# Kernel tuning notes

Measured on AMD Instinct MI355X. Metric: run time of the kernel, lower is better.

Reference implementation:

```python
import jax, jax.numpy as jnp
import numpy as np

N = 8192
DIN = 256
DOUT = 128
ALPHA = 0.2      # leaky-relu negative slope
K_MAX = 32       # static upper bound on action.max()+1 (action in [0, 32))
NEG_BIG = -9.0e15


def setup_inputs() -> dict:
    key = jax.random.key(0)
    ks = jax.random.split(key, 6)
    xavier_w = 1.414 * np.sqrt(6.0 / (DIN + DOUT))
    xavier_a = 1.414 * np.sqrt(6.0 / (DOUT + 1))
    return {
        "input": jax.random.normal(ks[0], (N, DIN), dtype=jnp.float32),
        "adj": jax.random.randint(ks[1], (N, N), 0, 2, dtype=jnp.int32),
        "action": jax.random.randint(ks[2], (N,), 0, K_MAX, dtype=jnp.int32),
        "W": jax.random.uniform(ks[3], (DIN, DOUT), jnp.float32, -xavier_w, xavier_w),
        "a_self": jax.random.uniform(ks[4], (DOUT, 1), jnp.float32, -xavier_a, xavier_a),
        "a_neighs": jax.random.uniform(ks[5], (DOUT, 1), jnp.float32, -xavier_a, xavier_a),
        "breadth_policy": 1,
    }


def reference(input, adj, action, W, a_self, a_neighs, breadth_policy):
    h = input @ W                                  # [N, DOUT]
    attn_self = h @ a_self                         # [N, 1]
    attn_neighs = h @ a_neighs                     # [N, 1]
    e = jax.nn.leaky_relu(attn_self + attn_neighs.T, negative_slope=ALPHA)  # [N, N]
    masked = jnp.where(adj > 0, e, jnp.float32(NEG_BIG))
    attention = jax.nn.softmax(masked, axis=1)     # [N, N]
    if breadth_policy:
        # static K_MAX >= action.max()+1; thresholds only read index action[i]
        top_vals, _ = jax.lax.top_k(attention, K_MAX)          # [N, K_MAX], sorted desc
        thresholds = top_vals[jnp.arange(N), action]           # [N]
        attention = jnp.where(attention < thresholds[:, None], 0.0, attention)
    h_prime = attention @ h                        # [N, DOUT]
    return jax.nn.elu(h_prime)                     # concat=True
```

## Files before the change

kernel.cpp:

```cpp
#include <hip/hip_runtime.h>
#include <cstdint>
#include <cstddef>

#define NN    8192
#define DIN   256
#define DOUT  128
#define LRA   0.2f

__global__ __launch_bounds__(256) void gemm_st_kernel(
    const float* __restrict__ input, const float* __restrict__ W,
    const float* __restrict__ a_self, const float* __restrict__ a_neighs,
    float* __restrict__ h, float* __restrict__ s_arr,
    float* __restrict__ t_arr)
{
    __shared__ float tile[16][DIN];
    __shared__ float pr[4][16];
    const int tid  = threadIdx.x;
    const int row0 = blockIdx.x * 16;
    {
        const float4* in4 = (const float4*)(input + (size_t)row0 * DIN);
        float4* t4 = (float4*)&tile[0][0];
        #pragma unroll
        for (int k = 0; k < 4; ++k) t4[tid + k * 256] = in4[tid + k * 256];
    }
    __syncthreads();
    const int c    = tid & 127;
    const int g    = tid >> 7;
    const int lane = tid & 63;
    const int wave = tid >> 6;
    float acc[8];
    #pragma unroll
    for (int m = 0; m < 8; ++m) acc[m] = 0.f;
    for (int k = 0; k < DIN; k += 4) {
        const float w0 = W[(k + 0) * DOUT + c];
        const float w1 = W[(k + 1) * DOUT + c];
        const float w2 = W[(k + 2) * DOUT + c];
        const float w3 = W[(k + 3) * DOUT + c];
        #pragma unroll
        for (int m = 0; m < 8; ++m) {
            const float4 av = *(const float4*)&tile[g * 8 + m][k];
            acc[m] += av.x * w0 + av.y * w1 + av.z * w2 + av.w * w3;
        }
    }
    #pragma unroll
    for (int m = 0; m < 8; ++m)
        h[(size_t)(row0 + g * 8 + m) * DOUT + c] = acc[m];

    const float as = a_self[c];
    const float an = a_neighs[c];
    #pragma unroll
    for (int m = 0; m < 8; ++m) {
        float vs = acc[m] * as;
        float vt = acc[m] * an;
        for (int off = 32; off > 0; off >>= 1) {
            vs += __shfl_down(vs, off);
            vt += __shfl_down(vt, off);
        }
        if (lane == 0) { pr[wave][2 * m] = vs; pr[wave][2 * m + 1] = vt; }
    }
    __syncthreads();
    if (tid < 16) {
        const int m  = tid & 7;
        const int gg = tid >> 3;
        const int r  = row0 + gg * 8 + m;
        s_arr[r] = pr[2 * gg][2 * m]     + pr[2 * gg + 1][2 * m];
        t_arr[r] = pr[2 * gg][2 * m + 1] + pr[2 * gg + 1][2 * m + 1];
    }
}

__global__ __launch_bounds__(256) void rank_kernel(
    const float* __restrict__ t, int* __restrict__ order,
    float* __restrict__ tsorted)
{
    __shared__ float tl[NN];
    __shared__ int   part[8][32];
    for (int k = threadIdx.x; k < NN; k += 256) tl[k] = t[k];
    __syncthreads();
    const int jloc = threadIdx.x & 31;
    const int seg  = threadIdx.x >> 5;
    const int j    = blockIdx.x * 32 + jloc;
    const float tj = tl[j];
    int r = 0;
    const int k0 = seg * (NN / 8);
    for (int i = 0; i < NN / 8; ++i) {
        const int k = k0 + ((i + seg * 4) & (NN / 8 - 1));
        const float tk = tl[k];
        r += (tk > tj || (tk == tj && k < j)) ? 1 : 0;
    }
    part[seg][jloc] = r;
    __syncthreads();
    if (threadIdx.x < 32) {
        int rr = 0;
        #pragma unroll
        for (int ss = 0; ss < 8; ++ss) rr += part[ss][threadIdx.x];
        const int jj = blockIdx.x * 32 + threadIdx.x;
        order[rr]   = jj;
        tsorted[rr] = tl[jj];
    }
}

__global__ __launch_bounds__(256) void gat_row_kernel(
    const int* __restrict__ adj, const float* __restrict__ s_arr,
    const float* __restrict__ t_arr, const int* __restrict__ order,
    const float* __restrict__ tsorted, const int* __restrict__ action,
    const float* __restrict__ h, const int* __restrict__ policy,
    float* __restrict__ out)
{
    __shared__ float red[4];
    __shared__ float numlds[8][DOUT];
    __shared__ unsigned long long maskb[32][4];
    __shared__ int   sel_j[64];
    __shared__ float sel_w[64];
    __shared__ int   sel_cnt_sh;
    __shared__ int   done_sh;

    const int row  = blockIdx.x;
    const int tid  = threadIdx.x;
    const int lane = tid & 63;
    const int wave = tid >> 6;

    const float s    = s_arr[row];
    const float tmax = tsorted[0];
    const float zc   = s + tmax;
    const float C    = fmaxf(zc, LRA * zc);

    const int4*   arow = (const int4*)(adj + (size_t)row * NN);
    const float4* t4   = (const float4*)t_arr;
    float acc = 0.f;
    #pragma unroll
    for (int k = 0; k < 8; ++k) {
        const int idx = tid + k * 256;
        const int4   a  = arow[idx];
        const float4 tv = t4[idx];
        const int vx = a.x > 0, vy = a.y > 0, vz = a.z > 0, vw = a.w > 0;
        float z, e;
        z = s + tv.x; e = fmaxf(z, LRA * z); if (vx) acc += __expf(e - C);
        z = s + tv.y; e = fmaxf(z, LRA * z); if (vy) acc += __expf(e - C);
        z = s + tv.z; e = fmaxf(z, LRA * z); if (vz) acc += __expf(e - C);
        z = s + tv.w; e = fmaxf(z, LRA * z); if (vw) acc += __expf(e - C);
        const unsigned long long b0 = __ballot(vx);
        const unsigned long long b1 = __ballot(vy);
        const unsigned long long b2 = __ballot(vz);
        const unsigned long long b3 = __ballot(vw);
        if (lane == 0) {
            const int ch = 4 * k + wave;
            maskb[ch][0] = b0; maskb[ch][1] = b1;
            maskb[ch][2] = b2; maskb[ch][3] = b3;
        }
    }
    for (int off = 32; off > 0; off >>= 1) acc += __shfl_down(acc, off);
    if (lane == 0) red[wave] = acc;
    __syncthreads();
    const float l = red[0] + red[1] + red[2] + red[3];

    int K = action[row] + 1;
    if (policy[0] == 0) K = 0x7FFFFFFF;
    const int ee = tid >> 5;
    const int c4 = tid & 31;
    float4 acc4 = make_float4(0.f, 0.f, 0.f, 0.f);
    float tthr = -3.0e38f;
    int found = 0, cnt = 0, base = 0;

    while (true) {
        if (tid < 64) {
            const int p = base + lane;
            int j = 0, valid = 0;
            float tjv = -3.0e38f;
            if (p < NN) {
                j     = order[p];
                tjv   = tsorted[p];
                valid = (int)((maskb[j >> 8][j & 3] >> ((j & 255) >> 2)) & 1ull);
            }
            const unsigned long long vm = __ballot(valid);
            if (!found) {
                const int cv = __popcll(vm);
                if (cnt + cv >= K) {
                    const int need = K - cnt;
                    const int myrank =
                        __popcll(vm & ((1ull << lane) - 1ull)) + 1;
                    const unsigned long long pm =
                        __ballot(valid && (myrank == need));
                    const int L = __ffsll((long long)pm) - 1;
                    tthr  = __shfl(tjv, L);
                    found = 1;
                } else {
                    cnt += cv;
                }
            }
            const int selected = valid && (tjv >= tthr);
            const unsigned long long sm = __ballot(selected);
            const int pos = __popcll(sm & ((1ull << lane) - 1ull));
            if (selected) {
                const float z = s + tjv;
                const float e = fmaxf(z, LRA * z);
                sel_j[pos] = j;
                sel_w[pos] = __expf(e - C);
            }
            if (lane == 0) {
                sel_cnt_sh = __popcll(sm);
                const int nb = base + 64;
                int dn;
                if (nb >= NN)   dn = 1;
                else if (found) dn = (tsorted[nb] < tthr) ? 1 : 0;
                else            dn = 0;
                done_sh = dn;
            }
        }
        __syncthreads();
        const int nsel = sel_cnt_sh;
        const int dn   = done_sh;
        for (int e2 = ee; e2 < nsel; e2 += 8) {
            const float w = sel_w[e2];
            const float4 hv =
                *(const float4*)&h[(size_t)sel_j[e2] * DOUT + c4 * 4];
            acc4.x += w * hv.x; acc4.y += w * hv.y;
            acc4.z += w * hv.z; acc4.w += w * hv.w;
        }
        base += 64;
        if (dn) break;
        __syncthreads();
    }

    *(float4*)&numlds[ee][c4 * 4] = acc4;
    __syncthreads();
    if (tid < DOUT) {
        float v = 0.f;
        #pragma unroll
        for (int q = 0; q < 8; ++q) v += numlds[q][tid];
        v /= l;
        out[(size_t)row * DOUT + tid] = (v > 0.f) ? v : expm1f(v);
    }
}

extern "C" void kernel_launch(void* const* d_in, const int* in_sizes, int n_in,
                              void* d_out, int out_size, void* d_ws,
                              size_t ws_size, hipStream_t stream)
{
    const float* input    = (const float*)d_in[0];
    const int*   adj      = (const int*)d_in[1];
    const int*   action   = (const int*)d_in[2];
    const float* W        = (const float*)d_in[3];
    const float* a_self   = (const float*)d_in[4];
    const float* a_neighs = (const float*)d_in[5];
    const int*   policy   = (const int*)d_in[6];
    float* out = (float*)d_out;

    float* ws      = (float*)d_ws;
    float* h       = ws;
    float* s       = ws + (size_t)NN * DOUT;
    float* t       = s + NN;
    float* tsorted = t + NN;
    int*   order   = (int*)(tsorted + NN);

    hipLaunchKernelGGL(gemm_st_kernel, dim3(512), dim3(256), 0, stream,
                       input, W, a_self, a_neighs, h, s, t);
    hipLaunchKernelGGL(rank_kernel, dim3(256), dim3(256), 0, stream,
                       t, order, tsorted);
    hipLaunchKernelGGL(gat_row_kernel, dim3(NN), dim3(256), 0, stream,
                       adj, s, t, order, tsorted, action, h, policy, out);
}
```

Before: 459.6 us.

## Split row kernel into denominator pass and one-wave-per-row top-k walk

The fused per-row kernel is split in two. The first kernel streams adj, computes the softmax denominator and writes the adjacency bitmask to global memory. The second kernel handles one row per 64-lane wave, using shuffles instead of LDS and block barriers, and walks the sorted candidates to gather h. The aim is to stop three idle waves per block from waiting on barriers during the serial walk. The cost is an extra launch plus a global round trip for the mask (8192x1KB) and the denominators.

```diff
diff --git a/kernel.cpp b/kernel.cpp
--- a/kernel.cpp
+++ b/kernel.cpp
@@ -99,21 +99,12 @@
     }
 }
 
-__global__ __launch_bounds__(256) void gat_row_kernel(
+__global__ __launch_bounds__(256) void denom_kernel(
     const int* __restrict__ adj, const float* __restrict__ s_arr,
-    const float* __restrict__ t_arr, const int* __restrict__ order,
-    const float* __restrict__ tsorted, const int* __restrict__ action,
-    const float* __restrict__ h, const int* __restrict__ policy,
-    float* __restrict__ out)
+    const float* __restrict__ t_arr, const float* __restrict__ tsorted,
+    float* __restrict__ denom, unsigned long long* __restrict__ mask)
 {
     __shared__ float red[4];
-    __shared__ float numlds[8][DOUT];
-    __shared__ unsigned long long maskb[32][4];
-    __shared__ int   sel_j[64];
-    __shared__ float sel_w[64];
-    __shared__ int   sel_cnt_sh;
-    __shared__ int   done_sh;
-
     const int row  = blockIdx.x;
     const int tid  = threadIdx.x;
     const int lane = tid & 63;
@@ -126,10 +117,12 @@
 
     const int4*   arow = (const int4*)(adj + (size_t)row * NN);
     const float4* t4   = (const float4*)t_arr;
+    unsigned long long* mrow = mask + (size_t)row * 128;
+
     float acc = 0.f;
     #pragma unroll
     for (int k = 0; k < 8; ++k) {
-        const int idx = tid + k * 256;
+        const int idx = tid + (k << 8);
         const int4   a  = arow[idx];
         const float4 tv = t4[idx];
         const int vx = a.x > 0, vy = a.y > 0, vz = a.z > 0, vw = a.w > 0;
@@ -142,94 +135,97 @@
         const unsigned long long b1 = __ballot(vy);
         const unsigned long long b2 = __ballot(vz);
         const unsigned long long b3 = __ballot(vw);
-        if (lane == 0) {
-            const int ch = 4 * k + wave;
-            maskb[ch][0] = b0; maskb[ch][1] = b1;
-            maskb[ch][2] = b2; maskb[ch][3] = b3;
+        if (lane < 4) {
+            const unsigned long long bv =
+                (lane == 0) ? b0 : (lane == 1) ? b1 : (lane == 2) ? b2 : b3;
+            mrow[(4 * k + wave) * 4 + lane] = bv;
         }
     }
     for (int off = 32; off > 0; off >>= 1) acc += __shfl_down(acc, off);
     if (lane == 0) red[wave] = acc;
     __syncthreads();
-    const float l = red[0] + red[1] + red[2] + red[3];
-
-    int K = action[row] + 1;
-    if (policy[0] == 0) K = 0x7FFFFFFF;
-    const int ee = tid >> 5;
-    const int c4 = tid & 31;
-    float4 acc4 = make_float4(0.f, 0.f, 0.f, 0.f);
+    if (tid == 0) denom[row] = red[0] + red[1] + red[2] + red[3];
+}
+
+__global__ __launch_bounds__(256) void walk_kernel(
+    const float* __restrict__ s_arr, const int* __restrict__ order,
+    const float* __restrict__ tsorted,
+    const unsigned long long* __restrict__ mask,
+    const float* __restrict__ denom, const int* __restrict__ action,
+    const float* __restrict__ h, const int* __restrict__ policy,
+    float* __restrict__ out)
+{
+    const int row  = (blockIdx.x * 256 + threadIdx.x) >> 6;
+    const int lane = threadIdx.x & 63;
+
+    const float s    = s_arr[row];
+    const float tmax = tsorted[0];
+    const float zc   = s + tmax;
+    const float C    = fmaxf(zc, LRA * zc);
+
+    const ulonglong2 mw =
+        *(const ulonglong2*)(mask + (size_t)row * 128 + 2 * lane);
+
+    int K = policy[0] ? (action[row] + 1) : 0x7FFFFFFF;
+
+    float2 acc = make_float2(0.f, 0.f);
     float tthr = -3.0e38f;
     int found = 0, cnt = 0, base = 0;
 
     while (true) {
-        if (tid < 64) {
-            const int p = base + lane;
-            int j = 0, valid = 0;
-            float tjv = -3.0e38f;
-            if (p < NN) {
-                j     = order[p];
-                tjv   = tsorted[p];
-                valid = (int)((maskb[j >> 8][j & 3] >> ((j & 255) >> 2)) & 1ull);
+        const int p    = base + lane;
+        const int j    = order[p];
+        const float tjv = tsorted[p];
+        const int W    = ((j >> 8) << 2) | (j & 3);
+        const int bit  = (j & 255) >> 2;
+        const unsigned long long wa = __shfl(mw.x, W >> 1);
+        const unsigned long long wb = __shfl(mw.y, W >> 1);
+        const unsigned long long word = (W & 1) ? wb : wa;
+        const int valid = (int)((word >> bit) & 1ull);
+
+        const unsigned long long vm = __ballot(valid);
+        if (!found) {
+            const int cv = __popcll(vm);
+            if (cnt + cv >= K) {
+                const int need   = K - cnt;
+                const int myrank = __popcll(vm & ((1ull << lane) - 1ull)) + 1;
+                const unsigned long long pm =
+                    __ballot(valid && (myrank == need));
+                const int L = __ffsll((long long)pm) - 1;
+                tthr  = __shfl(tjv, L);
+                found = 1;
+            } else {
+                cnt += cv;
             }
-            const unsigned long long vm = __ballot(valid);
-            if (!found) {
-                const int cv = __popcll(vm);
-                if (cnt + cv >= K) {
-                    const int need = K - cnt;
-                    const int myrank =
-                        __popcll(vm & ((1ull << lane) - 1ull)) + 1;
-                    const unsigned long long pm =
-                        __ballot(valid && (myrank == need));
-                    const int L = __ffsll((long long)pm) - 1;
-                    tthr  = __shfl(tjv, L);
-                    found = 1;
-                } else {
-                    cnt += cv;
-                }
-            }
-            const int selected = valid && (tjv >= tthr);
-            const unsigned long long sm = __ballot(selected);
-            const int pos = __popcll(sm & ((1ull << lane) - 1ull));
-            if (selected) {
-                const float z = s + tjv;
-                const float e = fmaxf(z, LRA * z);
-                sel_j[pos] = j;
-                sel_w[pos] = __expf(e - C);
-            }
-            if (lane == 0) {
-                sel_cnt_sh = __popcll(sm);
-                const int nb = base + 64;
-                int dn;
-                if (nb >= NN)   dn = 1;
-                else if (found) dn = (tsorted[nb] < tthr) ? 1 : 0;
-                else            dn = 0;
-                done_sh = dn;
-            }
-        }
-        __syncthreads();
-        const int nsel = sel_cnt_sh;
-        const int dn   = done_sh;
-        for (int e2 = ee; e2 < nsel; e2 += 8) {
-            const float w = sel_w[e2];
-            const float4 hv =
-                *(const float4*)&h[(size_t)sel_j[e2] * DOUT + c4 * 4];
-            acc4.x += w * hv.x; acc4.y += w * hv.y;
-            acc4.z += w * hv.z; acc4.w += w * hv.w;
+        }
+        const int selected = valid && (tjv >= tthr);
+        float wv = 0.f;
+        if (selected) {
+            const float z = s + tjv;
+            const float e = fmaxf(z, LRA * z);
+            wv = __expf(e - C);
+        }
+        unsigned long long sm = __ballot(selected);
+        while (sm) {
+            const int L = __ffsll((long long)sm) - 1;
+            sm &= sm - 1ull;
+            const int   jj = __shfl(j, L);
+            const float w  = __shfl(wv, L);
+            const float2 hv =
+                *(const float2*)&h[(size_t)jj * DOUT + 2 * lane];
+            acc.x += w * hv.x;
+            acc.y += w * hv.y;
         }
         base += 64;
-        if (dn) break;
-        __syncthreads();
-    }
-
-    *(float4*)&numlds[ee][c4 * 4] = acc4;
-    __syncthreads();
-    if (tid < DOUT) {
-        float v = 0.f;
-        #pragma unroll
-        for (int q = 0; q < 8; ++q) v += numlds[q][tid];
-        v /= l;
-        out[(size_t)row * DOUT + tid] = (v > 0.f) ? v : expm1f(v);
-    }
+        if (base >= NN) break;
+        if (found && tsorted[base] < tthr) break;
+    }
+
+    const float linv = 1.f / denom[row];
+    float vx = acc.x * linv, vy = acc.y * linv;
+    vx = (vx > 0.f) ? vx : expm1f(vx);
+    vy = (vy > 0.f) ? vy : expm1f(vy);
+    *(float2*)&out[(size_t)row * DOUT + 2 * lane] = make_float2(vx, vy);
 }
 
 extern "C" void kernel_launch(void* const* d_in, const int* in_sizes, int n_in,
@@ -250,12 +246,17 @@
     float* s       = ws + (size_t)NN * DOUT;
     float* t       = s + NN;
     float* tsorted = t + NN;
-    int*   order   = (int*)(tsorted + NN);
+    float* denom   = tsorted + NN;
+    int*   order   = (int*)(denom + NN);
+    unsigned long long* mask =
+        (unsigned long long*)(order + NN);
 
     hipLaunchKernelGGL(gemm_st_kernel, dim3(512), dim3(256), 0, stream,
                        input, W, a_self, a_neighs, h, s, t);
     hipLaunchKernelGGL(rank_kernel, dim3(256), dim3(256), 0, stream,
                        t, order, tsorted);
-    hipLaunchKernelGGL(gat_row_kernel, dim3(NN), dim3(256), 0, stream,
-                       adj, s, t, order, tsorted, action, h, policy, out);
-}
+    hipLaunchKernelGGL(denom_kernel, dim3(NN), dim3(256), 0, stream,
+                       adj, s, t, tsorted, denom, mask);
+    hipLaunchKernelGGL(walk_kernel, dim3(NN / 4), dim3(256), 0, stream,
+                       s, order, tsorted, mask, denom, action, h, policy, out);
+}
```

Result: no change. 465.9 us (+1.4%).
